# Kernel optimization log

Hardware: AMD Instinct MI355X
Metric: run time of the kernel (lower is better)

Reference implementation:

```python
import jax, jax.numpy as jnp
import numpy as np

CHEB_K = 2  # hops per support; stacked terms = 1 + 2*CHEB_K = 5


def setup_inputs() -> dict:
    key = jax.random.key(0)
    k1, k2, k3, k4, k5 = jax.random.split(key, 5)
    B, N, C, O, D = 16, 1024, 64, 64, 10
    return {
        "x": jax.random.normal(k1, (B, N, C), dtype=jnp.float32),
        "adj": jax.random.uniform(k2, (2, B, N, N), dtype=jnp.float32),
        "node_embedding": jax.random.normal(k3, (N, D), dtype=jnp.float32),
        "weights_pool": jax.random.normal(k4, (D, 2 * CHEB_K + 1, C, O), dtype=jnp.float32) * 0.1,
        "bias_pool": jax.random.normal(k5, (D, O), dtype=jnp.float32) * 0.1,
    }


def reference(x, adj, node_embedding, weights_pool, bias_pool):
    # k-hop graph aggregation over each of the 2 supports
    out = [x]
    for s in range(adj.shape[0]):
        a = adj[s]  # [B, N, N]
        x1 = x
        for _ in range(CHEB_K):
            x1 = jnp.einsum('bnm,bmc->bnc', a, x1)
            out.append(x1)
    x_g = jnp.stack(out, axis=2)  # [B, N, K, C] with K = 2*cheb_k+1 (already node-major)
    # per-node hypernetwork weights and bias from node embeddings
    weights = jnp.einsum('nd,dkio->nkio', node_embedding, weights_pool)  # [N, K, C, O]
    bias = node_embedding @ bias_pool  # [N, O]
    # per-node contraction over (K, C)
    return jnp.einsum('bnki,nkio->bno', x_g, weights) + bias
```

## Files before the change

### kernel.cpp

```cpp
#include <hip/hip_runtime.h>
#include <stdint.h>


typedef __attribute__((ext_vector_type(4))) float f32x4;
typedef __attribute__((ext_vector_type(2))) float f32x2;
typedef __attribute__((ext_vector_type(8))) short s16x8;
typedef __attribute__((ext_vector_type(8))) __bf16 bf16x8;

__device__ __forceinline__ unsigned short f2bf(float f) {
  union { float f; uint32_t u; } v; v.f = f;
  uint32_t r = v.u + 0x7FFFu + ((v.u >> 16) & 1u);
  return (unsigned short)(r >> 16);
}
__device__ __forceinline__ uint32_t pack2(float a, float b) {
  return (uint32_t)f2bf(a) | ((uint32_t)f2bf(b) << 16);
}

union FragU { s16x8 s; bf16x8 b; };

__device__ __forceinline__ void async_cp16(const void* g, void* l) {
  __builtin_amdgcn_global_load_lds(
      (const __attribute__((address_space(1))) void*)g,
      (__attribute__((address_space(3))) void*)l, 16, 0, 0);
}

__global__ void transpose_x(const float* __restrict__ x,
                            unsigned short* __restrict__ XT0) {
  __shared__ unsigned short tl[64][72];
  const int b = blockIdx.y, n0 = blockIdx.x * 64;
  const int tid = threadIdx.x;
  {
    const int c4 = (tid & 15) * 4;
#pragma unroll
    for (int i = 0; i < 4; ++i) {
      const int row = (tid >> 4) + i * 16;
      f32x4 v = *(const f32x4*)(x + ((size_t)(b * 1024 + n0 + row)) * 64 + c4);
      *(uint32_t*)&tl[row][c4]     = pack2(v[0], v[1]);
      *(uint32_t*)&tl[row][c4 + 2] = pack2(v[2], v[3]);
    }
  }
  __syncthreads();
  {
    const int c = tid >> 2;
    const int nch = (tid & 3) * 16;
    s16x8 s0, s1;
#pragma unroll
    for (int j = 0; j < 8; ++j) {
      s0[j] = (short)tl[nch + j][c];
      s1[j] = (short)tl[nch + 8 + j][c];
    }
    unsigned short* p = XT0 + (size_t)(b * 64 + c) * 1024 + n0 + nch;
    *(s16x8*)p = s0;
    *(s16x8*)(p + 8) = s1;
  }
}

__global__ void transpose_wp(const float* __restrict__ wp,
                             float* __restrict__ wpT) {
  __shared__ float tl[64][65];
  const int d = blockIdx.y;
  const int ki0 = blockIdx.x * 64;
  const int tid = threadIdx.x;
  const float* src = wp + (size_t)d * 20480;
  {
    const int o4 = (tid & 15) * 4;
#pragma unroll
    for (int i = 0; i < 4; ++i) {
      const int row = (tid >> 4) + i * 16;
      f32x4 v = *(const f32x4*)(src + (size_t)(ki0 + row) * 64 + o4);
      tl[row][o4] = v[0]; tl[row][o4 + 1] = v[1];
      tl[row][o4 + 2] = v[2]; tl[row][o4 + 3] = v[3];
    }
  }
  __syncthreads();
  {
    const int o = tid >> 2;
    const int kch = (tid & 3) * 16;
    float* dst = wpT + (size_t)d * 20480 + (size_t)o * 320 + ki0 + kch;
#pragma unroll
    for (int u = 0; u < 4; ++u) {
      f32x4 v = { tl[kch + 4 * u][o], tl[kch + 4 * u + 1][o],
                  tl[kch + 4 * u + 2][o], tl[kch + 4 * u + 3][o] };
      *(f32x4*)(dst + 4 * u) = v;
    }
  }
}

__global__ __launch_bounds__(256) void wgen(const float* __restrict__ wpT,
                                            const float* __restrict__ emb,
                                            unsigned short* __restrict__ WT) {
  const int idx = (blockIdx.x * 256 + threadIdx.x) * 2;
  const int n0 = blockIdx.y * 16;
  f32x2 wv[10];
#pragma unroll
  for (int d = 0; d < 10; ++d)
    wv[d] = *(const f32x2*)(wpT + (size_t)d * 20480 + idx);
#pragma unroll
  for (int g = 0; g < 16; ++g) {
    float a0 = 0.f, a1 = 0.f;
#pragma unroll
    for (int d = 0; d < 10; ++d) {
      const float e = emb[(n0 + g) * 10 + d];
      a0 += e * wv[d][0];
      a1 += e * wv[d][1];
    }
    *(uint32_t*)(WT + (size_t)(n0 + g) * 20480 + idx) = pack2(a0, a1);
  }
}

__global__ __launch_bounds__(256, 2) void hop_kernel(
    const float* __restrict__ adj, const unsigned short* __restrict__ XTin,
    float* __restrict__ Xout, unsigned short* __restrict__ XTout,
    int xt_shared, int write_xt) {
  __shared__ __align__(16) char smem[2 * (16384 + 8192)];
  const int slice = blockIdx.y;
  const int b = slice & 15;
  const float* __restrict__ A = adj + (size_t)slice * (1024u * 1024u);
  const unsigned short* __restrict__ XT =
      XTin + (size_t)(xt_shared ? b : slice) * (64 * 1024);
  const int tid = threadIdx.x;
  const int wave = tid >> 6, lane = tid & 63;
  const int l15 = lane & 15, q = lane >> 4;
  const int rowbase = blockIdx.x * 64;

  int arow[4], acol[4];
#pragma unroll
  for (int i = 0; i < 4; ++i) {
    const int r = wave * 16 + i * 4 + (lane >> 4);
    arow[i] = r;
    acol[i] = ((lane & 15) ^ (r & 7)) * 4;
  }
  int bc[2], bcol[2];
#pragma unroll
  for (int i = 0; i < 2; ++i) {
    const int c = wave * 16 + i * 8 + (lane >> 3);
    bc[i] = c;
    bcol[i] = ((lane & 7) ^ (c & 7)) * 8;
  }

  float* const Ab0 = (float*)smem;
  float* const Ab1 = (float*)(smem + 24576);
  unsigned short* const Bb0 = (unsigned short*)(smem + 16384);
  unsigned short* const Bb1 = (unsigned short*)(smem + 24576 + 16384);

  auto issue = [&](int k0, int s) {
    float* Abuf = s ? Ab1 : Ab0;
    unsigned short* Bbuf = s ? Bb1 : Bb0;
#pragma unroll
    for (int i = 0; i < 4; ++i)
      async_cp16(A + (size_t)(rowbase + arow[i]) * 1024 + k0 + acol[i],
                 Abuf + (size_t)(wave * 16 + i * 4) * 64);
#pragma unroll
    for (int i = 0; i < 2; ++i)
      async_cp16(XT + (size_t)bc[i] * 1024 + k0 + bcol[i],
                 Bbuf + (size_t)(wave * 16 + i * 8) * 64);
  };

  f32x4 acc[4];
#pragma unroll
  for (int t = 0; t < 4; ++t) acc[t] = (f32x4){0.f, 0.f, 0.f, 0.f};

  issue(0, 0);
  const int r = wave * 16 + l15;
  const int rx = r & 7;
  for (int kt = 0; kt < 16; ++kt) {
    const int cur = kt & 1;
    __syncthreads();
    if (kt + 1 < 16) issue((kt + 1) * 64, cur ^ 1);
    const float* Abuf = cur ? Ab1 : Ab0;
    const unsigned short* Bbuf = cur ? Bb1 : Bb0;
#pragma unroll
    for (int h = 0; h < 2; ++h) {
      const int j0 = h * 8 + q * 2;
      f32x4 c0 = *(const f32x4*)(Abuf + r * 64 + ((j0) ^ rx) * 4);
      f32x4 c1 = *(const f32x4*)(Abuf + r * 64 + ((j0 + 1) ^ rx) * 4);
      FragU af;
#pragma unroll
      for (int e = 0; e < 4; ++e) {
        af.s[e]     = (short)f2bf(c0[e]);
        af.s[e + 4] = (short)f2bf(c1[e]);
      }
      const int pc = (h * 4 + q) ^ (l15 & 7);
#pragma unroll
      for (int t = 0; t < 4; ++t) {
        FragU bf;
        bf.s = *(const s16x8*)(Bbuf + (t * 16 + l15) * 64 + pc * 8);
        acc[t] = __builtin_amdgcn_mfma_f32_16x16x32_bf16(af.b, bf.b, acc[t],
                                                         0, 0, 0);
      }
    }
  }

  __syncthreads();
  float (*tile)[65] = (float(*)[65])smem;
#pragma unroll
  for (int t = 0; t < 4; ++t)
#pragma unroll
    for (int rr = 0; rr < 4; ++rr)
      tile[wave * 16 + q * 4 + rr][t * 16 + l15] = acc[t][rr];
  __syncthreads();

  {
    const int row = tid >> 2;
    const int cb = (tid & 3) * 16;
    float* __restrict__ outp = Xout + (size_t)slice * (1024 * 64) +
                               (size_t)(rowbase + row) * 64 + cb;
#pragma unroll
    for (int u = 0; u < 4; ++u) {
      f32x4 v = { tile[row][cb + 4 * u], tile[row][cb + 4 * u + 1],
                  tile[row][cb + 4 * u + 2], tile[row][cb + 4 * u + 3] };
      *(f32x4*)(outp + 4 * u) = v;
    }
  }
  if (write_xt) {
    const int c = tid >> 2;
    const int nch = (tid & 3) * 16;
    unsigned short* __restrict__ xtp = XTout + (size_t)slice * (64 * 1024) +
                                       (size_t)c * 1024 + rowbase + nch;
    s16x8 s0, s1;
#pragma unroll
    for (int j = 0; j < 8; ++j) {
      s0[j] = (short)f2bf(tile[nch + j][c]);
      s1[j] = (short)f2bf(tile[nch + 8 + j][c]);
    }
    *(s16x8*)xtp = s0;
    *(s16x8*)(xtp + 8) = s1;
  }
}

__global__ __launch_bounds__(256, 2) void final_kernel(
    const float* __restrict__ x, const float* __restrict__ X1,
    const float* __restrict__ X2, const unsigned short* __restrict__ WT,
    const float* __restrict__ emb, const float* __restrict__ bias_pool,
    float* __restrict__ out) {
  __shared__ unsigned short xg[4][16][328];
  const int tid = threadIdx.x;
  const int node_base = blockIdx.x * 4;

  for (int u = tid; u < 10240; u += 256) {
    const int nd = u / 2560;
    int rem = u - nd * 2560;
    const int bb = rem / 160;
    const int kiu = rem - bb * 160;
    const int ki = kiu * 2;
    const int k = ki >> 6;
    const int c = ki & 63;
    const int nn = node_base + nd;
    const float* src;
    if (k == 0) {
      src = x + ((size_t)bb * 1024 + nn) * 64 + c;
    } else {
      const float* arr = (k == 1 || k == 3) ? X1 : X2;
      const int s = (k >= 3) ? 1 : 0;
      src = arr + ((size_t)(s * 16 + bb) * 1024 + nn) * 64 + c;
    }
    f32x2 v = *(const f32x2*)src;
    *(uint32_t*)&xg[nd][bb][ki] = pack2(v[0], v[1]);
  }
  __syncthreads();

  const int wave = tid >> 6, lane = tid & 63;
  const int l15 = lane & 15, q = lane >> 4;
  const int n = node_base + wave;
  f32x4 acc[4];
#pragma unroll
  for (int t = 0; t < 4; ++t) acc[t] = (f32x4){0.f, 0.f, 0.f, 0.f};

  const unsigned short* wt0 =
      WT + (size_t)n * 20480 + (size_t)l15 * 320 + q * 8;
#pragma unroll
  for (int ks = 0; ks < 10; ++ks) {
    const int k0 = ks * 32;
    FragU af;
    af.s = *(const s16x8*)&xg[wave][l15][k0 + q * 8];
#pragma unroll
    for (int t = 0; t < 4; ++t) {
      FragU bf;
      bf.s = *(const s16x8*)(wt0 + (size_t)t * (16 * 320) + k0);
      acc[t] = __builtin_amdgcn_mfma_f32_16x16x32_bf16(af.b, bf.b, acc[t],
                                                       0, 0, 0);
    }
  }

#pragma unroll
  for (int t = 0; t < 4; ++t) {
    const int o = t * 16 + l15;
    float bv = 0.f;
#pragma unroll
    for (int d = 0; d < 10; ++d)
      bv += emb[n * 10 + d] * bias_pool[d * 64 + o];
#pragma unroll
    for (int rr = 0; rr < 4; ++rr) {
      const int bb = q * 4 + rr;
      out[((size_t)bb * 1024 + n) * 64 + o] = acc[t][rr] + bv;
    }
  }
}

extern "C" void kernel_launch(void* const* d_in, const int* in_sizes, int n_in,
                              void* d_out, int out_size, void* d_ws,
                              size_t ws_size, hipStream_t stream) {
  const float* x   = (const float*)d_in[0];
  const float* adj = (const float*)d_in[1];
  const float* emb = (const float*)d_in[2];
  const float* wp  = (const float*)d_in[3];
  const float* bp  = (const float*)d_in[4];
  float* out = (float*)d_out;

  char* ws = (char*)d_ws;
  unsigned short* XT0 = (unsigned short*)(ws);
  unsigned short* XT1 = (unsigned short*)(ws + ((size_t)2 << 20));
  float* X1  = (float*)(ws + ((size_t)6 << 20));
  float* X2  = (float*)(ws + ((size_t)14 << 20));
  float* wpT = (float*)(ws + ((size_t)22 << 20));
  unsigned short* WT = (unsigned short*)(ws + ((size_t)23 << 20));

  transpose_x<<<dim3(16, 16), dim3(256), 0, stream>>>(x, XT0);
  transpose_wp<<<dim3(5, 10), dim3(256), 0, stream>>>(wp, wpT);
  wgen<<<dim3(40, 64), dim3(256), 0, stream>>>(wpT, emb, WT);
  hop_kernel<<<dim3(16, 32), dim3(256), 0, stream>>>(adj, XT0, X1, XT1, 1, 1);
  hop_kernel<<<dim3(16, 32), dim3(256), 0, stream>>>(adj, XT1, X2,
                                                     (unsigned short*)nullptr,
                                                     0, 0);
  final_kernel<<<dim3(256), dim3(256), 0, stream>>>(x, X1, X2, WT, emb, bp,
                                                    out);
}
```

Baseline: 279.1 us.

## Use per-wave register-pipelined hop kernel, reversed second pass, and split final kernel

```diff
diff --git a/kernel.cpp b/kernel.cpp
--- a/kernel.cpp
+++ b/kernel.cpp
@@ -23,6 +23,10 @@
       (const __attribute__((address_space(1))) void*)g,
       (__attribute__((address_space(3))) void*)l, 16, 0, 0);
 }
+
+#define WAITVM(n)                                                         \
+  __builtin_amdgcn_s_waitcnt(((n) & 15) | ((((n) >> 4) & 3) << 14) |      \
+                             (7 << 4) | (15 << 8))
 
 __global__ void transpose_x(const float* __restrict__ x,
                             unsigned short* __restrict__ XT0) {
@@ -111,9 +115,10 @@
 __global__ __launch_bounds__(256, 2) void hop_kernel(
     const float* __restrict__ adj, const unsigned short* __restrict__ XTin,
     float* __restrict__ Xout, unsigned short* __restrict__ XTout,
-    int xt_shared, int write_xt) {
-  __shared__ __align__(16) char smem[2 * (16384 + 8192)];
-  const int slice = blockIdx.y;
+    int xt_shared, int write_xt, int rev) {
+  __shared__ __align__(16) char smem[32768];
+  const int bx = rev ? (15 - (int)blockIdx.x) : (int)blockIdx.x;
+  const int slice = rev ? (31 - (int)blockIdx.y) : (int)blockIdx.y;
   const int b = slice & 15;
   const float* __restrict__ A = adj + (size_t)slice * (1024u * 1024u);
   const unsigned short* __restrict__ XT =
@@ -121,75 +126,77 @@
   const int tid = threadIdx.x;
   const int wave = tid >> 6, lane = tid & 63;
   const int l15 = lane & 15, q = lane >> 4;
-  const int rowbase = blockIdx.x * 64;
-
-  int arow[4], acol[4];
+  const int rowbase = bx * 64;
+
+  float* const Abase = (float*)smem + wave * 2048;
+
+  const float* ag[4];
 #pragma unroll
   for (int i = 0; i < 4; ++i) {
-    const int r = wave * 16 + i * 4 + (lane >> 4);
-    arow[i] = r;
-    acol[i] = ((lane & 15) ^ (r & 7)) * 4;
-  }
-  int bc[2], bcol[2];
-#pragma unroll
-  for (int i = 0; i < 2; ++i) {
-    const int c = wave * 16 + i * 8 + (lane >> 3);
-    bc[i] = c;
-    bcol[i] = ((lane & 7) ^ (c & 7)) * 8;
-  }
-
-  float* const Ab0 = (float*)smem;
-  float* const Ab1 = (float*)(smem + 24576);
-  unsigned short* const Bb0 = (unsigned short*)(smem + 16384);
-  unsigned short* const Bb1 = (unsigned short*)(smem + 24576 + 16384);
-
-  auto issue = [&](int k0, int s) {
-    float* Abuf = s ? Ab1 : Ab0;
-    unsigned short* Bbuf = s ? Bb1 : Bb0;
+    const int wl = i * 4 + (lane >> 4);
+    const int ch = (lane & 15) ^ (wl & 7);
+    ag[i] = A + (size_t)(rowbase + wave * 16 + wl) * 1024 + ch * 4;
+  }
+  const unsigned short* bg[8];
+#pragma unroll
+  for (int t = 0; t < 4; ++t)
+#pragma unroll
+    for (int h = 0; h < 2; ++h)
+      bg[t * 2 + h] = XT + (size_t)(t * 16 + l15) * 1024 + h * 32 + q * 8;
+
+  f32x4 acc[4];
+#pragma unroll
+  for (int t = 0; t < 4; ++t) acc[t] = (f32x4){0.f, 0.f, 0.f, 0.f};
+
+  s16x8 breg0[8], breg1[8];
+
+  auto issueA = [&](int k0, int s) {
 #pragma unroll
     for (int i = 0; i < 4; ++i)
-      async_cp16(A + (size_t)(rowbase + arow[i]) * 1024 + k0 + acol[i],
-                 Abuf + (size_t)(wave * 16 + i * 4) * 64);
-#pragma unroll
-    for (int i = 0; i < 2; ++i)
-      async_cp16(XT + (size_t)bc[i] * 1024 + k0 + bcol[i],
-                 Bbuf + (size_t)(wave * 16 + i * 8) * 64);
+      async_cp16(ag[i] + k0, Abase + s * 1024 + i * 256);
   };
-
-  f32x4 acc[4];
-#pragma unroll
-  for (int t = 0; t < 4; ++t) acc[t] = (f32x4){0.f, 0.f, 0.f, 0.f};
-
-  issue(0, 0);
-  const int r = wave * 16 + l15;
-  const int rx = r & 7;
-  for (int kt = 0; kt < 16; ++kt) {
-    const int cur = kt & 1;
-    __syncthreads();
-    if (kt + 1 < 16) issue((kt + 1) * 64, cur ^ 1);
-    const float* Abuf = cur ? Ab1 : Ab0;
-    const unsigned short* Bbuf = cur ? Bb1 : Bb0;
+  auto issueB = [&](int k0, s16x8 (&br)[8]) {
+#pragma unroll
+    for (int j = 0; j < 8; ++j) br[j] = *(const s16x8*)(bg[j] + k0);
+  };
+  auto compute = [&](int s, const s16x8 (&br)[8]) {
+    const float* Ab = Abase + s * 1024;
+    const int sw = l15 & 7;
 #pragma unroll
     for (int h = 0; h < 2; ++h) {
       const int j0 = h * 8 + q * 2;
-      f32x4 c0 = *(const f32x4*)(Abuf + r * 64 + ((j0) ^ rx) * 4);
-      f32x4 c1 = *(const f32x4*)(Abuf + r * 64 + ((j0 + 1) ^ rx) * 4);
+      f32x4 c0 = *(const f32x4*)(Ab + l15 * 64 + (j0 ^ sw) * 4);
+      f32x4 c1 = *(const f32x4*)(Ab + l15 * 64 + ((j0 + 1) ^ sw) * 4);
       FragU af;
 #pragma unroll
       for (int e = 0; e < 4; ++e) {
         af.s[e]     = (short)f2bf(c0[e]);
         af.s[e + 4] = (short)f2bf(c1[e]);
       }
-      const int pc = (h * 4 + q) ^ (l15 & 7);
 #pragma unroll
       for (int t = 0; t < 4; ++t) {
-        FragU bf;
-        bf.s = *(const s16x8*)(Bbuf + (t * 16 + l15) * 64 + pc * 8);
+        FragU bf; bf.s = br[t * 2 + h];
         acc[t] = __builtin_amdgcn_mfma_f32_16x16x32_bf16(af.b, bf.b, acc[t],
                                                          0, 0, 0);
       }
     }
-  }
+  };
+
+  issueA(0, 0);    issueB(0, breg0);
+  issueA(64, 1);   issueB(64, breg1);
+#pragma unroll 1
+  for (int kt = 0; kt < 14; kt += 2) {
+    WAITVM(12);
+    compute(0, breg0);
+    issueA((kt + 2) * 64, 0); issueB((kt + 2) * 64, breg0);
+    WAITVM(12);
+    compute(1, breg1);
+    issueA((kt + 3) * 64, 1); issueB((kt + 3) * 64, breg1);
+  }
+  WAITVM(12);
+  compute(0, breg0);
+  WAITVM(0);
+  compute(1, breg1);
 
   __syncthreads();
   float (*tile)[65] = (float(*)[65])smem;
@@ -233,11 +240,11 @@
     const float* __restrict__ X2, const unsigned short* __restrict__ WT,
     const float* __restrict__ emb, const float* __restrict__ bias_pool,
     float* __restrict__ out) {
-  __shared__ unsigned short xg[4][16][328];
+  __shared__ unsigned short xg[2][16][328];
   const int tid = threadIdx.x;
-  const int node_base = blockIdx.x * 4;
-
-  for (int u = tid; u < 10240; u += 256) {
+  const int node_base = blockIdx.x * 2;
+
+  for (int u = tid; u < 5120; u += 256) {
     const int nd = u / 2560;
     int rem = u - nd * 2560;
     const int bb = rem / 160;
@@ -260,11 +267,12 @@
   __syncthreads();
 
   const int wave = tid >> 6, lane = tid & 63;
+  const int nd = wave >> 1, oh = wave & 1;
   const int l15 = lane & 15, q = lane >> 4;
-  const int n = node_base + wave;
-  f32x4 acc[4];
-#pragma unroll
-  for (int t = 0; t < 4; ++t) acc[t] = (f32x4){0.f, 0.f, 0.f, 0.f};
+  const int n = node_base + nd;
+  f32x4 acc[2];
+#pragma unroll
+  for (int t = 0; t < 2; ++t) acc[t] = (f32x4){0.f, 0.f, 0.f, 0.f};
 
   const unsigned short* wt0 =
       WT + (size_t)n * 20480 + (size_t)l15 * 320 + q * 8;
@@ -272,19 +280,20 @@
   for (int ks = 0; ks < 10; ++ks) {
     const int k0 = ks * 32;
     FragU af;
-    af.s = *(const s16x8*)&xg[wave][l15][k0 + q * 8];
-#pragma unroll
-    for (int t = 0; t < 4; ++t) {
+    af.s = *(const s16x8*)&xg[nd][l15][k0 + q * 8];
+#pragma unroll
+    for (int tt = 0; tt < 2; ++tt) {
+      const int t = oh * 2 + tt;
       FragU bf;
       bf.s = *(const s16x8*)(wt0 + (size_t)t * (16 * 320) + k0);
-      acc[t] = __builtin_amdgcn_mfma_f32_16x16x32_bf16(af.b, bf.b, acc[t],
-                                                       0, 0, 0);
-    }
-  }
-
-#pragma unroll
-  for (int t = 0; t < 4; ++t) {
-    const int o = t * 16 + l15;
+      acc[tt] = __builtin_amdgcn_mfma_f32_16x16x32_bf16(af.b, bf.b, acc[tt],
+                                                        0, 0, 0);
+    }
+  }
+
+#pragma unroll
+  for (int tt = 0; tt < 2; ++tt) {
+    const int o = (oh * 2 + tt) * 16 + l15;
     float bv = 0.f;
 #pragma unroll
     for (int d = 0; d < 10; ++d)
@@ -292,7 +301,7 @@
 #pragma unroll
     for (int rr = 0; rr < 4; ++rr) {
       const int bb = q * 4 + rr;
-      out[((size_t)bb * 1024 + n) * 64 + o] = acc[t][rr] + bv;
+      out[((size_t)bb * 1024 + n) * 64 + o] = acc[tt][rr] + bv;
     }
   }
 }
@@ -316,12 +325,13 @@
   unsigned short* WT = (unsigned short*)(ws + ((size_t)23 << 20));
 
   transpose_x<<<dim3(16, 16), dim3(256), 0, stream>>>(x, XT0);
+  hop_kernel<<<dim3(16, 32), dim3(256), 0, stream>>>(adj, XT0, X1, XT1,
+                                                     1, 1, 0);
+  hop_kernel<<<dim3(16, 32), dim3(256), 0, stream>>>(adj, XT1, X2,
+                                                     (unsigned short*)nullptr,
+                                                     0, 0, 1);
   transpose_wp<<<dim3(5, 10), dim3(256), 0, stream>>>(wp, wpT);
   wgen<<<dim3(40, 64), dim3(256), 0, stream>>>(wpT, emb, WT);
-  hop_kernel<<<dim3(16, 32), dim3(256), 0, stream>>>(adj, XT0, X1, XT1, 1, 1);
-  hop_kernel<<<dim3(16, 32), dim3(256), 0, stream>>>(adj, XT1, X2,
-                                                     (unsigned short*)nullptr,
-                                                     0, 0);
-  final_kernel<<<dim3(256), dim3(256), 0, stream>>>(x, X1, X2, WT, emb, bp,
+  final_kernel<<<dim3(512), dim3(256), 0, stream>>>(x, X1, X2, WT, emb, bp,
                                                     out);
 }
```

New measurement: 283.0 us. Within noise of the previous version (+1.4%).
